# Optimization experiments

Measured on AMD Instinct MI355X. Metric: run time of the kernel, lower is better.

## Reference

```python
import jax, jax.numpy as jnp
import numpy as np

NB_FEATURES = 128
ACCUMULATION = 4


def iterative_inv(mat, n_iter=6):
    # Newton-Schulz iteration for matrix inverse ('original' init: global max)
    I = jnp.eye(mat.shape[-1], dtype=mat.dtype)
    K = mat
    V = (1.0 / jnp.max(jnp.sum(K, axis=-2))) * jnp.swapaxes(K, -1, -2)
    for _ in range(n_iter):
        KV = K @ V
        V = 0.25 * V @ (13.0 * I - KV @ (15.0 * I - KV @ (7.0 * I - KV)))
    return V


def setup_inputs() -> dict:
    key = jax.random.key(0)
    kq, kk, kv, ks = jax.random.split(key, 4)
    b, h, n, d = 4, 8, 2048, 64
    q = jax.random.normal(kq, (b, h, n, d), dtype=jnp.float32)
    k = jax.random.normal(kk, (b, h, n, d), dtype=jnp.float32)
    v = jax.random.normal(kv, (b, h, n, d), dtype=jnp.float32)
    mask = jnp.ones((b, n), dtype=jnp.float32)
    total = ACCUMULATION * NB_FEATURES
    # uniform_sketching: indices in [0,n) scaled by non_padding_num (=n here),
    # second half of the flat index list offset by +n to index the k-block of X.
    S = jax.random.randint(ks, (b, total), 0, n)
    S = S.at[:, total // 2:].add(n)
    sketching_matrix = S.reshape(b, ACCUMULATION, NB_FEATURES)
    random_sign = jnp.ones((b, ACCUMULATION, NB_FEATURES), dtype=jnp.float32)
    return {"q": q, "k": k, "v": v, "mask": mask,
            "random_sign": random_sign, "sketching_matrix": sketching_matrix}


def reference(q, k, v, mask, random_sign, sketching_matrix):
    b, h, n, d = q.shape
    data_normalizer = 32.0 ** (-0.25)
    m = mask[:, None, :, None]                      # [b,1,n,1]
    q = q * (m * data_normalizer)
    k = k * (m * data_normalizer)
    v = v * m

    X = jnp.concatenate([q, k], axis=2)             # [b,h,2n,d]
    Xt = jnp.transpose(X, (0, 2, 1, 3))             # [b,2n,h,d]
    XS = Xt[jnp.arange(b)[:, None, None], sketching_matrix]  # [b,acc,f,h,d]
    XS = jnp.transpose(XS, (0, 3, 1, 2, 4))         # [b,h,acc,f,d]

    # RS-RBF kernel sketch: exp(x.y - |x|^2/2 - |y|^2/2), accumulated over acc
    diag1 = (0.5 * jnp.sum(X * X, axis=-1))[:, :, None, :, None]   # [b,h,1,2n,1]
    diag2 = (0.5 * jnp.sum(XS * XS, axis=-1))[:, :, :, None, :]    # [b,h,acc,1,f]
    prod = jnp.einsum('bhnp,bhmfp->bhmnf', X, XS) - diag1 - diag2  # [b,h,acc,2n,f]
    res = jnp.exp(prod)
    res = jnp.transpose(res, (0, 1, 3, 2, 4))       # [b,h,2n,acc,f]
    AS = jnp.einsum('bhnmf,bmf->bhnf', res, random_sign)  # [b,h,2n,f]

    Q = AS[:, :, :n]                                # [b,h,n,f]
    K = AS[:, :, n:]                                # [b,h,n,f]

    ASt = jnp.transpose(AS, (0, 2, 1, 3))           # [b,2n,h,f]
    STAS = ASt[jnp.arange(b)[:, None, None], sketching_matrix]     # [b,acc,f,h,f]
    STAS = jnp.einsum('bmdhe,bmd->bhde', STAS, random_sign)        # [b,h,f,f]
    f = STAS.shape[-1]
    STAS = STAS + 0.1 * jnp.eye(f, dtype=STAS.dtype)

    D_inv = jnp.sqrt(1.0 / jnp.sum(STAS, axis=-1))  # [b,h,f]
    STAS_n = D_inv[..., :, None] * STAS * D_inv[..., None, :]
    STAS_inv = iterative_inv(STAS_n, 6)

    K = (K * D_inv[:, :, None, :]) @ STAS_inv       # [b,h,n,f]
    K = K * D_inv[:, :, None, :] * m

    context = jnp.einsum('bhnf,bhne->bhfe', K, v)   # [b,h,f,d]
    out = Q @ context                               # [b,h,n,d]
    return out
```

## Files before the change

kernel.cpp:

```cpp
#include <hip/hip_runtime.h>

constexpr int Bc = 4, Hc = 8, Nc = 2048, Dc = 64, Fc = 128, Mc = 4;
constexpr int BHc = Bc*Hc;
constexpr int T2c = 2*Nc;
constexpr int Jc  = Mc*Fc;
constexpr float DNORM = 0.4204482076268573f;

constexpr size_t OFF_AS    = 0;
constexpr size_t OFF_XSH   = OFF_AS    + (size_t)BHc*T2c*Fc;
constexpr size_t OFF_XSM   = OFF_XSH   + (size_t)BHc*Jc*Dc/2;
constexpr size_t OFF_XSL   = OFF_XSM   + (size_t)BHc*Jc*Dc/2;
constexpr size_t OFF_DIAG1 = OFF_XSL   + (size_t)BHc*Jc*Dc/2;
constexpr size_t OFF_DIAG2 = OFF_DIAG1 + (size_t)BHc*T2c;
constexpr size_t OFF_STASN = OFF_DIAG2 + (size_t)BHc*Jc;
constexpr size_t OFF_VBUF  = OFF_STASN + (size_t)BHc*Fc*Fc;
constexpr size_t OFF_DINV  = OFF_VBUF  + (size_t)BHc*Fc*Fc;
constexpr size_t OFF_GMAX  = OFF_DINV  + (size_t)BHc*Fc;
constexpr size_t OFF_CTX   = OFF_GMAX  + 64;
constexpr size_t OFF_KH    = OFF_CTX   + (size_t)BHc*Fc*Dc;
constexpr size_t OFF_KM    = OFF_KH    + (size_t)BHc*Fc*Fc/2;
constexpr size_t OFF_KL    = OFF_KM    + (size_t)BHc*Fc*Fc/2;
constexpr size_t OFF_GPART = OFF_XSH;
constexpr size_t OFF_ZSC   = OFF_GPART + (size_t)BHc*4*128*64;

typedef __attribute__((ext_vector_type(8))) short bf16x8;
typedef __attribute__((ext_vector_type(4))) float f32x4;
typedef __attribute__((ext_vector_type(4))) unsigned short u16x4;

__device__ __forceinline__ unsigned short f2bf_rne(float x) {
  unsigned int u = __float_as_uint(x);
  u += 0x7fff + ((u >> 16) & 1);
  return (unsigned short)(u >> 16);
}
__device__ __forceinline__ float bf2f(unsigned short h) {
  return __uint_as_float(((unsigned int)h) << 16);
}

__global__ __launch_bounds__(256) void diag1_kernel(
    const float* __restrict__ q, const float* __restrict__ k,
    const float* __restrict__ mask, float* __restrict__ diag1) {
  int gid = blockIdx.x*256 + threadIdx.x;
  int kq  = gid & 15;
  int row = gid >> 4;
  int t   = row & (T2c - 1);
  int bh  = row >> 12;
  int b   = bh >> 3;
  int tn  = (t < Nc) ? t : t - Nc;
  const float* src = ((t < Nc) ? q : k) + ((size_t)bh*Nc + tn)*Dc;
  float sc = DNORM * mask[b*Nc + tn];
  float4 x = *(const float4*)(src + kq*4);
  float s = x.x*x.x + x.y*x.y + x.z*x.z + x.w*x.w;
  s += __shfl_xor(s, 1);
  s += __shfl_xor(s, 2);
  s += __shfl_xor(s, 4);
  s += __shfl_xor(s, 8);
  if (kq == 0) diag1[row] = 0.5f * sc * sc * s;
}

__global__ __launch_bounds__(256) void gather_kernel(
    const float* __restrict__ q, const float* __restrict__ k,
    const float* __restrict__ mask, const int* __restrict__ sketch,
    const float* __restrict__ diag1,
    unsigned short* __restrict__ xsh, unsigned short* __restrict__ xsm,
    unsigned short* __restrict__ xsl, float* __restrict__ diag2) {
  int gid = blockIdx.x*256 + threadIdx.x;
  int kq  = gid & 15;
  int idx = gid >> 4;
  int j   = idx & (Jc - 1);
  int bh  = idx >> 9;
  int b   = bh >> 3;
  int t   = sketch[b*Jc + j];
  int tn  = (t < Nc) ? t : t - Nc;
  const float* src = ((t < Nc) ? q : k) + ((size_t)bh*Nc + tn)*Dc;
  float sc = DNORM * mask[b*Nc + tn];
  float4 x = *(const float4*)(src + kq*4);
  float xv[4] = {x.x*sc, x.y*sc, x.z*sc, x.w*sc};
  u16x4 hh, mm_, ll;
  #pragma unroll
  for (int jj = 0; jj < 4; ++jj) {
    unsigned short h = f2bf_rne(xv[jj]);
    float r1 = xv[jj] - bf2f(h);
    unsigned short m = f2bf_rne(r1);
    float r2 = r1 - bf2f(m);
    hh[jj] = h; mm_[jj] = m; ll[jj] = f2bf_rne(r2);
  }
  *(u16x4*)(xsh + (size_t)idx*Dc + kq*4) = hh;
  *(u16x4*)(xsm + (size_t)idx*Dc + kq*4) = mm_;
  *(u16x4*)(xsl + (size_t)idx*Dc + kq*4) = ll;
  if (kq == 0) diag2[idx] = diag1[bh*T2c + t];
}

__global__ __launch_bounds__(256) void as_mfma_kernel(
    const float* __restrict__ q, const float* __restrict__ k,
    const float* __restrict__ mask,
    const unsigned short* __restrict__ xsh, const unsigned short* __restrict__ xsm,
    const unsigned short* __restrict__ xsl,
    const float* __restrict__ diag1, const float* __restrict__ diag2,
    const float* __restrict__ sign, float* __restrict__ AS) {
  __shared__ __align__(16) unsigned short Ah[64][72];
  __shared__ __align__(16) unsigned short Am[64][72];
  __shared__ __align__(16) unsigned short Al[64][72];
  __shared__ float d1s[64];
  __shared__ float d2s[4][128];
  __shared__ float sgs[4][128];
  int bh = blockIdx.y, b = bh >> 3;
  int t0 = blockIdx.x * 64;
  int tid = threadIdx.x;
  int lane = tid & 63, wid = tid >> 6;
  int wr = wid >> 1, wc = wid & 1;
  int l16 = lane & 15, lg = lane >> 4;
  int R0 = wr*32, C0 = wc*64;

  for (int i = tid; i < 64*16; i += 256) {
    int r = i >> 4, kq = i & 15;
    int t = t0 + r;
    int tn = (t < Nc) ? t : t - Nc;
    const float* src = ((t < Nc) ? q : k) + ((size_t)bh*Nc + tn)*Dc + kq*4;
    float sc = DNORM * mask[b*Nc + tn];
    float4 x = *(const float4*)src;
    float xv[4] = {x.x*sc, x.y*sc, x.z*sc, x.w*sc};
    u16x4 hv, mv, lv;
    #pragma unroll
    for (int jj = 0; jj < 4; ++jj) {
      unsigned short h = f2bf_rne(xv[jj]);
      float r1 = xv[jj] - bf2f(h);
      unsigned short m = f2bf_rne(r1);
      float r2 = r1 - bf2f(m);
      hv[jj] = h; mv[jj] = m; lv[jj] = f2bf_rne(r2);
    }
    *(u16x4*)&Ah[r][kq*4] = hv;
    *(u16x4*)&Am[r][kq*4] = mv;
    *(u16x4*)&Al[r][kq*4] = lv;
  }
  if (tid < 64) d1s[tid] = diag1[bh*T2c + t0 + tid];
  for (int i = tid; i < 512; i += 256) {
    d2s[i>>7][i&127] = diag2[bh*Jc + i];
    sgs[i>>7][i&127] = sign[b*Jc + i];
  }
  __syncthreads();

  const unsigned short* xhh = xsh + (size_t)bh*Jc*Dc;
  const unsigned short* xmm = xsm + (size_t)bh*Jc*Dc;
  const unsigned short* xll = xsl + (size_t)bh*Jc*Dc;
  f32x4 oa[2][4];
  #pragma unroll
  for (int m = 0; m < 2; ++m)
    #pragma unroll
    for (int n = 0; n < 4; ++n) oa[m][n] = 0.f;

  for (int m = 0; m < Mc; ++m) {
    f32x4 acc[2][4];
    #pragma unroll
    for (int mm = 0; mm < 2; ++mm)
      #pragma unroll
      for (int nn = 0; nn < 4; ++nn) acc[mm][nn] = 0.f;
    #pragma unroll
    for (int kc = 0; kc < Dc; kc += 32) {
      int ko = kc + lg*8;
      bf16x8 ah[2], am2[2], al2[2], bhv[4], bmv[4], blv[4];
      #pragma unroll
      for (int mm = 0; mm < 2; ++mm) {
        ah[mm]  = *(const bf16x8*)&Ah[R0+16*mm+l16][ko];
        am2[mm] = *(const bf16x8*)&Am[R0+16*mm+l16][ko];
        al2[mm] = *(const bf16x8*)&Al[R0+16*mm+l16][ko];
      }
      #pragma unroll
      for (int nn = 0; nn < 4; ++nn) {
        size_t p = (size_t)(m*Fc + C0 + 16*nn + l16)*Dc + ko;
        bhv[nn] = *(const bf16x8*)(xhh + p);
        bmv[nn] = *(const bf16x8*)(xmm + p);
        blv[nn] = *(const bf16x8*)(xll + p);
      }
      #pragma unroll
      for (int mm = 0; mm < 2; ++mm)
        #pragma unroll
        for (int nn = 0; nn < 4; ++nn) {
          acc[mm][nn] = __builtin_amdgcn_mfma_f32_16x16x32_bf16(am2[mm], bmv[nn], acc[mm][nn], 0,0,0);
          acc[mm][nn] = __builtin_amdgcn_mfma_f32_16x16x32_bf16(ah[mm],  blv[nn], acc[mm][nn], 0,0,0);
          acc[mm][nn] = __builtin_amdgcn_mfma_f32_16x16x32_bf16(al2[mm], bhv[nn], acc[mm][nn], 0,0,0);
          acc[mm][nn] = __builtin_amdgcn_mfma_f32_16x16x32_bf16(ah[mm],  bmv[nn], acc[mm][nn], 0,0,0);
          acc[mm][nn] = __builtin_amdgcn_mfma_f32_16x16x32_bf16(am2[mm], bhv[nn], acc[mm][nn], 0,0,0);
          acc[mm][nn] = __builtin_amdgcn_mfma_f32_16x16x32_bf16(ah[mm],  bhv[nn], acc[mm][nn], 0,0,0);
        }
    }
    #pragma unroll
    for (int mm = 0; mm < 2; ++mm)
      #pragma unroll
      for (int nn = 0; nn < 4; ++nn) {
        int c = C0 + 16*nn + l16;
        float d2v = d2s[m][c], sg = sgs[m][c];
        #pragma unroll
        for (int r = 0; r < 4; ++r) {
          int row = R0 + 16*mm + 4*lg + r;
          oa[mm][nn][r] += sg * __expf(acc[mm][nn][r] - d1s[row] - d2v);
        }
      }
  }
  #pragma unroll
  for (int mm = 0; mm < 2; ++mm)
    #pragma unroll
    for (int nn = 0; nn < 4; ++nn) {
      int c = C0 + 16*nn + l16;
      #pragma unroll
      for (int r = 0; r < 4; ++r) {
        int row = R0 + 16*mm + 4*lg + r;
        AS[((size_t)bh*T2c + t0 + row)*Fc + c] = oa[mm][nn][r];
      }
    }
}

__global__ __launch_bounds__(256) void stas_kernel(
    const float* __restrict__ AS, const int* __restrict__ sketch,
    const float* __restrict__ sign,
    float* __restrict__ STASn, float* __restrict__ Dinv,
    unsigned short* __restrict__ Kh, unsigned short* __restrict__ Km,
    unsigned short* __restrict__ Kl,
    unsigned int* __restrict__ gmax) {
  extern __shared__ float stas[];
  __shared__ int   Ssh[Jc];
  __shared__ float sgn[Jc];
  __shared__ float Dl[Fc];
  __shared__ float red[Fc];
  int bh = blockIdx.x;
  int b  = bh >> 3;
  int tid = threadIdx.x;
  for (int i = tid; i < Jc; i += 256) {
    Ssh[i] = sketch[b*Jc + i];
    sgn[i] = sign[b*Jc + i];
  }
  __syncthreads();
  for (int i = tid; i < Fc*Fc; i += 256) {
    int dd = i >> 7, e = i & 127;
    float vsum = 0.f;
    #pragma unroll
    for (int m = 0; m < Mc; ++m) {
      int t = Ssh[m*Fc + dd];
      vsum += sgn[m*Fc + dd] * AS[((size_t)bh*T2c + t)*Fc + e];
    }
    if (dd == e) vsum += 0.1f;
    stas[dd*129 + e] = vsum;
  }
  __syncthreads();
  if (tid < Fc) {
    float s = 0.f;
    for (int e = 0; e < Fc; ++e) s += stas[tid*129 + e];
    float di = 1.0f / sqrtf(s);
    Dl[tid] = di;
    Dinv[bh*Fc + tid] = di;
  }
  __syncthreads();
  for (int i = tid; i < Fc*Fc; i += 256) {
    int dd = i >> 7, e = i & 127;
    float vv = stas[dd*129 + e] * Dl[dd] * Dl[e];
    stas[dd*129 + e] = vv;
    STASn[(size_t)bh*Fc*Fc + i] = vv;
    unsigned short hb = f2bf_rne(vv); float r1 = vv - bf2f(hb);
    unsigned short mb = f2bf_rne(r1); float r2 = r1 - bf2f(mb);
    Kh[(size_t)bh*Fc*Fc + i] = hb;
    Km[(size_t)bh*Fc*Fc + i] = mb;
    Kl[(size_t)bh*Fc*Fc + i] = f2bf_rne(r2);
  }
  __syncthreads();
  if (tid < Fc) {
    float s = 0.f;
    for (int dd = 0; dd < Fc; ++dd) s += stas[dd*129 + tid];
    red[tid] = s;
  }
  __syncthreads();
  if (tid == 0) {
    float mx = 0.f;
    for (int e = 0; e < Fc; ++e) mx = fmaxf(mx, red[e]);
    atomicMax(gmax, __float_as_uint(mx));
  }
}

__device__ __forceinline__ unsigned boff(int brow, int ke) {
  unsigned byte = ((unsigned)brow << 8) | ((unsigned)ke << 1);
  return byte ^ (((unsigned)(brow & 7)) << 4);
}

__device__ __forceinline__ void mm6(const bf16x8 ah[2], const bf16x8 am[2], const bf16x8 al[2],
                                    const bf16x8 bh[4], const bf16x8 bm[4], const bf16x8 bl[4],
                                    f32x4 acc[2][4]) {
  #pragma unroll
  for (int m = 0; m < 2; ++m)
    #pragma unroll
    for (int n = 0; n < 4; ++n) {
      acc[m][n] = __builtin_amdgcn_mfma_f32_16x16x32_bf16(am[m], bm[n], acc[m][n], 0,0,0);
      acc[m][n] = __builtin_amdgcn_mfma_f32_16x16x32_bf16(ah[m], bl[n], acc[m][n], 0,0,0);
      acc[m][n] = __builtin_amdgcn_mfma_f32_16x16x32_bf16(al[m], bh[n], acc[m][n], 0,0,0);
      acc[m][n] = __builtin_amdgcn_mfma_f32_16x16x32_bf16(ah[m], bm[n], acc[m][n], 0,0,0);
      acc[m][n] = __builtin_amdgcn_mfma_f32_16x16x32_bf16(am[m], bh[n], acc[m][n], 0,0,0);
      acc[m][n] = __builtin_amdgcn_mfma_f32_16x16x32_bf16(ah[m], bh[n], acc[m][n], 0,0,0);
    }
}

__device__ __forceinline__ void ld3(const char* Ph, const char* Pm, const char* Pl,
                                    int brow, int ko, bf16x8& h, bf16x8& m, bf16x8& l) {
  unsigned off = boff(brow, ko);
  h = *(const bf16x8*)(Ph + off);
  m = *(const bf16x8*)(Pm + off);
  l = *(const bf16x8*)(Pl + off);
}

__device__ __forceinline__ void mm_p1(
    const unsigned short* __restrict__ kh, const unsigned short* __restrict__ km,
    const unsigned short* __restrict__ kl,
    const char* Ah, const char* Am, const char* Al,
    int R0, int C0, int l16, int lg, f32x4 acc[2][4]) {
  #pragma unroll 1
  for (int kc = 0; kc < Fc; kc += 32) {
    int ko = kc + lg*8;
    bf16x8 ah[2], am[2], al[2], bh[4], bm[4], bl[4];
    #pragma unroll
    for (int m = 0; m < 2; ++m) {
      size_t p = (size_t)(R0+16*m+l16)*Fc + ko;
      ah[m] = *(const bf16x8*)(kh + p);
      am[m] = *(const bf16x8*)(km + p);
      al[m] = *(const bf16x8*)(kl + p);
    }
    #pragma unroll
    for (int n = 0; n < 4; ++n)
      ld3(Ah, Am, Al, C0+16*n+l16, ko, bh[n], bm[n], bl[n]);
    mm6(ah, am, al, bh, bm, bl, acc);
  }
}

__device__ __forceinline__ void mm_p234(
    const char* Ah, const char* Am, const char* Al,
    const char* Zh, const char* Zm, const unsigned short* __restrict__ ZlG,
    int R0, int C0, int l16, int lg, f32x4 acc[2][4]) {
  #pragma unroll 1
  for (int kc = 0; kc < Fc; kc += 32) {
    int ko = kc + lg*8;
    bf16x8 ah[2], am[2], al[2], bh[4], bm[4], bl[4];
    #pragma unroll
    for (int m = 0; m < 2; ++m)
      ld3(Ah, Am, Al, R0+16*m+l16, ko, ah[m], am[m], al[m]);
    #pragma unroll
    for (int n = 0; n < 4; ++n) {
      int col = C0+16*n+l16;
      unsigned off = boff(col, ko);
      bh[n] = *(const bf16x8*)(Zh + off);
      bm[n] = *(const bf16x8*)(Zm + off);
      bl[n] = *(const bf16x8*)(ZlG + col*Fc + ko);
    }
    mm6(ah, am, al, bh, bm, bl, acc);
  }
}

__device__ __forceinline__ void split4(f32x4 v, u16x4& hv, u16x4& mv, u16x4& lv) {
  #pragma unroll
  for (int r = 0; r < 4; ++r) {
    unsigned short hb = f2bf_rne(v[r]); float r1 = v[r] - bf2f(hb);
    unsigned short mb = f2bf_rne(r1);   float r2 = r1 - bf2f(mb);
    hv[r] = hb; mv[r] = mb; lv[r] = f2bf_rne(r2);
  }
}
__device__ __forceinline__ void wbA3(char* Ah, char* Am, char* Al,
                                     int col, int row0, f32x4 v) {
  u16x4 hv, mv, lv;
  split4(v, hv, mv, lv);
  unsigned off = boff(col, row0);
  *(u16x4*)(Ah + off) = hv;
  *(u16x4*)(Am + off) = mv;
  *(u16x4*)(Al + off) = lv;
}
__device__ __forceinline__ void wbZ3(char* Zh, char* Zm, unsigned short* __restrict__ ZlG,
                                     int col, int row0, f32x4 v) {
  u16x4 hv, mv, lv;
  split4(v, hv, mv, lv);
  unsigned off = boff(col, row0);
  *(u16x4*)(Zh + off) = hv;
  *(u16x4*)(Zm + off) = mv;
  *(u16x4*)(ZlG + col*Fc + row0) = lv;
}

__global__ __launch_bounds__(512) void newton_ctx_kernel(
    const float* __restrict__ STASn,
    const unsigned short* __restrict__ KhG, const unsigned short* __restrict__ KmG,
    const unsigned short* __restrict__ KlG,
    const float* __restrict__ gmaxf, float* __restrict__ Vout,
    const float* __restrict__ ASg, const float* __restrict__ vg,
    const float* __restrict__ maskg, float* __restrict__ Gpart,
    unsigned short* __restrict__ ZlScr) {
  extern __shared__ char smc[];
  int tid  = threadIdx.x;

  if (blockIdx.x < BHc) {
    char* Ah = smc;
    char* Am = smc + 32768;
    char* Al = smc + 65536;
    char* Zh = smc + 98304;
    char* Zm = smc + 131072;
    int bh = blockIdx.x;
    const float* Kp = STASn + (size_t)bh*Fc*Fc;
    const unsigned short* kh = KhG + (size_t)bh*Fc*Fc;
    const unsigned short* km = KmG + (size_t)bh*Fc*Fc;
    const unsigned short* kl = KlG + (size_t)bh*Fc*Fc;
    unsigned short* ZlG = ZlScr + (size_t)bh*Fc*Fc;
    float ginv = 1.0f / gmaxf[0];
    int lane = tid & 63;
    int wid  = tid >> 6;
    int wr = wid >> 1, wc = wid & 1;
    int l16 = lane & 15, lg = lane >> 4;
    int R0 = wr*32, C0 = wc*64;
    int drow0 = lg*4;

    f32x4 vreg[2][4];
    #pragma unroll
    for (int m = 0; m < 2; ++m)
      #pragma unroll
      for (int n = 0; n < 4; ++n) {
        int col = C0 + 16*n + l16;
        #pragma unroll
        for (int r = 0; r < 4; ++r)
          vreg[m][n][r] = Kp[(size_t)(R0 + 16*m + drow0 + r)*Fc + col] * ginv;
        wbA3(Ah, Am, Al, col, R0 + 16*m + drow0, vreg[m][n]);
      }
    __syncthreads();

    f32x4 fin[2][4];
    for (int it = 0; it < 6; ++it) {
      f32x4 acc[2][4];
      #pragma unroll
      for (int m = 0; m < 2; ++m) for (int n = 0; n < 4; ++n) acc[m][n] = 0.f;
      mm_p1(kh, km, kl, Ah, Am, Al, R0, C0, l16, lg, acc);
      #pragma unroll
      for (int m = 0; m < 2; ++m)
        #pragma unroll
        for (int n = 0; n < 4; ++n)
          wbZ3(Zh, Zm, ZlG, C0 + 16*n + l16, R0 + 16*m + drow0, acc[m][n]);
      __syncthreads();

      #pragma unroll
      for (int m = 0; m < 2; ++m) for (int n = 0; n < 4; ++n) acc[m][n] = 0.f;
      mm_p234(Ah, Am, Al, Zh, Zm, ZlG, R0, C0, l16, lg, acc);
      #pragma unroll
      for (int m = 0; m < 2; ++m)
        #pragma unroll
        for (int n = 0; n < 4; ++n)
          fin[m][n] = 13.f*vreg[m][n] - 15.f*acc[m][n];
      __syncthreads();
      #pragma unroll
      for (int m = 0; m < 2; ++m)
        #pragma unroll
        for (int n = 0; n < 4; ++n)
          wbA3(Ah, Am, Al, C0 + 16*n + l16, R0 + 16*m + drow0, acc[m][n]);
      __syncthreads();

      #pragma unroll
      for (int m = 0; m < 2; ++m) for (int n = 0; n < 4; ++n) acc[m][n] = 0.f;
      mm_p234(Ah, Am, Al, Zh, Zm, ZlG, R0, C0, l16, lg, acc);
      #pragma unroll
      for (int m = 0; m < 2; ++m)
        #pragma unroll
        for (int n = 0; n < 4; ++n)
          fin[m][n] += 7.f*acc[m][n];
      __syncthreads();
      #pragma unroll
      for (int m = 0; m < 2; ++m)
        #pragma unroll
        for (int n = 0; n < 4; ++n)
          wbA3(Ah, Am, Al, C0 + 16*n + l16, R0 + 16*m + drow0, acc[m][n]);
      __syncthreads();

      #pragma unroll
      for (int m = 0; m < 2; ++m) for (int n = 0; n < 4; ++n) acc[m][n] = 0.f;
      mm_p234(Ah, Am, Al, Zh, Zm, ZlG, R0, C0, l16, lg, acc);
      #pragma unroll
      for (int m = 0; m < 2; ++m)
        #pragma unroll
        for (int n = 0; n < 4; ++n) {
          fin[m][n] = 0.25f*(fin[m][n] - acc[m][n]);
          vreg[m][n] = fin[m][n];
        }
      __syncthreads();
      #pragma unroll
      for (int m = 0; m < 2; ++m)
        #pragma unroll
        for (int n = 0; n < 4; ++n)
          wbA3(Ah, Am, Al, C0 + 16*n + l16, R0 + 16*m + drow0, fin[m][n]);
      __syncthreads();
    }

    float* Vo = Vout + (size_t)bh*Fc*Fc;
    #pragma unroll
    for (int m = 0; m < 2; ++m)
      #pragma unroll
      for (int n = 0; n < 4; ++n) {
        int col = C0 + 16*n + l16;
        #pragma unroll
        for (int r = 0; r < 4; ++r)
          Vo[(size_t)(R0 + 16*m + drow0 + r)*Fc + col] = vreg[m][n][r];
      }
  } else {
    float* Ksh = (float*)smc;
    float* vsh = (float*)(smc + 32768);
    int id = blockIdx.x - BHc;
    int cbh = id >> 2, chunk = id & 3;
    int cb = cbh >> 3;
    int t0 = chunk * 512;
    int f = tid & 127, g = tid >> 7;
    float acc[16];
    #pragma unroll
    for (int j = 0; j < 16; ++j) acc[j] = 0.f;
    for (int sub = 0; sub < 8; ++sub) {
      __syncthreads();
      int ts = t0 + sub*64;
      for (int i = tid; i < 64*32; i += 512) {
        int r = i >> 5, c4 = i & 31;
        *(float4*)&Ksh[r*128 + c4*4] =
            *(const float4*)(ASg + ((size_t)cbh*T2c + Nc + ts + r)*Fc + c4*4);
      }
      for (int i = tid; i < 64*16; i += 512) {
        int r = i >> 4, c4 = i & 15;
        float mk = maskg[cb*Nc + ts + r];
        float m2 = mk*mk;
        float4 x = *(const float4*)(vg + ((size_t)cbh*Nc + ts + r)*Dc + c4*4);
        x.x*=m2; x.y*=m2; x.z*=m2; x.w*=m2;
        *(float4*)&vsh[r*64 + c4*4] = x;
      }
      __syncthreads();
      #pragma unroll 2
      for (int tl = 0; tl < 64; ++tl) {
        float kf = Ksh[tl*128 + f];
        #pragma unroll
        for (int j4 = 0; j4 < 4; ++j4) {
          float4 vv = *(const float4*)&vsh[tl*64 + g*16 + j4*4];
          acc[j4*4+0] += kf*vv.x; acc[j4*4+1] += kf*vv.y;
          acc[j4*4+2] += kf*vv.z; acc[j4*4+3] += kf*vv.w;
        }
      }
    }
    float* gp = Gpart + ((((size_t)cbh*4 + chunk)*128 + f)*64 + g*16);
    #pragma unroll
    for (int j4 = 0; j4 < 4; ++j4)
      *(float4*)(gp + j4*4) = *(const float4*)&acc[j4*4];
  }
}

__global__ __launch_bounds__(256) void ctx_fix_kernel(
    const float* __restrict__ Gpart, const float* __restrict__ Vinv,
    const float* __restrict__ Dinv, float* __restrict__ ctxo) {
  __shared__ float DG[128*64];
  __shared__ float Dl[128];
  int bh = blockIdx.x;
  int tid = threadIdx.x;
  if (tid < 128) Dl[tid] = Dinv[bh*Fc + tid];
  __syncthreads();
  for (int i = tid; i < 2048; i += 256) {
    int e = i >> 4, c4 = i & 15;
    const float* g0 = Gpart + ((((size_t)bh*4)*128 + e)*64 + c4*4);
    float4 s0 = *(const float4*)(g0);
    float4 s1 = *(const float4*)(g0 + 8192);
    float4 s2 = *(const float4*)(g0 + 16384);
    float4 s3 = *(const float4*)(g0 + 24576);
    float de = Dl[e];
    float4 o;
    o.x = (s0.x+s1.x+s2.x+s3.x)*de;
    o.y = (s0.y+s1.y+s2.y+s3.y)*de;
    o.z = (s0.z+s1.z+s2.z+s3.z)*de;
    o.w = (s0.w+s1.w+s2.w+s3.w)*de;
    *(float4*)&DG[e*64 + c4*4] = o;
  }
  __syncthreads();
  int f = tid & 127, half = tid >> 7;
  float acc[32];
  #pragma unroll
  for (int j = 0; j < 32; ++j) acc[j] = 0.f;
  for (int e = 0; e < 128; ++e) {
    float s = Vinv[(size_t)bh*Fc*Fc + (size_t)e*Fc + f];
    #pragma unroll
    for (int j4 = 0; j4 < 8; ++j4) {
      float4 dg = *(const float4*)&DG[e*64 + half*32 + j4*4];
      acc[j4*4+0] += s*dg.x; acc[j4*4+1] += s*dg.y;
      acc[j4*4+2] += s*dg.z; acc[j4*4+3] += s*dg.w;
    }
  }
  float df = Dl[f];
  float* op = ctxo + (size_t)bh*Fc*Dc + f*Dc + half*32;
  #pragma unroll
  for (int j4 = 0; j4 < 8; ++j4) {
    float4 o;
    o.x = acc[j4*4+0]*df; o.y = acc[j4*4+1]*df;
    o.z = acc[j4*4+2]*df; o.w = acc[j4*4+3]*df;
    *(float4*)(op + j4*4) = o;
  }
}

__global__ __launch_bounds__(256) void out_kernel(
    const float* __restrict__ AS, const float* __restrict__ ctx,
    float* __restrict__ out) {
  extern __shared__ float smo[];
  float* Asq = smo;
  float* Cs  = smo + 64*132;
  int bh = blockIdx.y;
  int row0 = blockIdx.x * 64;
  int tid = threadIdx.x;
  int tr = tid >> 4, tc = tid & 15;
  for (int i = tid; i < 64*32; i += 256) {
    int r = i >> 5, kq = i & 31;
    *(float4*)&Asq[r*132 + kq*4] =
        *(const float4*)(AS + ((size_t)bh*T2c + row0 + r)*Fc + kq*4);
  }
  for (int i = tid; i < 128*16; i += 256) {
    int r = i >> 4, kq = i & 15;
    *(float4*)&Cs[r*64 + kq*4] =
        *(const float4*)(ctx + (size_t)bh*Fc*Dc + r*Dc + kq*4);
  }
  __syncthreads();
  float acc[4][4] = {};
  #pragma unroll 2
  for (int kk = 0; kk < Fc; ++kk) {
    float4 bv = *(const float4*)&Cs[kk*64 + tc*4];
    float a0 = Asq[(tr*4+0)*132 + kk];
    float a1 = Asq[(tr*4+1)*132 + kk];
    float a2 = Asq[(tr*4+2)*132 + kk];
    float a3 = Asq[(tr*4+3)*132 + kk];
    acc[0][0] += a0*bv.x; acc[0][1] += a0*bv.y; acc[0][2] += a0*bv.z; acc[0][3] += a0*bv.w;
    acc[1][0] += a1*bv.x; acc[1][1] += a1*bv.y; acc[1][2] += a1*bv.z; acc[1][3] += a1*bv.w;
    acc[2][0] += a2*bv.x; acc[2][1] += a2*bv.y; acc[2][2] += a2*bv.z; acc[2][3] += a2*bv.w;
    acc[3][0] += a3*bv.x; acc[3][1] += a3*bv.y; acc[3][2] += a3*bv.z; acc[3][3] += a3*bv.w;
  }
  #pragma unroll
  for (int i = 0; i < 4; ++i) {
    float4 o;
    o.x = acc[i][0]; o.y = acc[i][1]; o.z = acc[i][2]; o.w = acc[i][3];
    *(float4*)(out + ((size_t)bh*Nc + row0 + tr*4 + i)*Dc + tc*4) = o;
  }
}

extern "C" void kernel_launch(void* const* d_in, const int* in_sizes, int n_in,
                              void* d_out, int out_size, void* d_ws, size_t ws_size,
                              hipStream_t stream) {
  const float* q    = (const float*)d_in[0];
  const float* k    = (const float*)d_in[1];
  const float* v    = (const float*)d_in[2];
  const float* mask = (const float*)d_in[3];
  const float* sign = (const float*)d_in[4];
  const int*   sketch = (const int*)d_in[5];
  float* out = (float*)d_out;
  float* ws  = (float*)d_ws;

  unsigned short* xsh = (unsigned short*)(ws + OFF_XSH);
  unsigned short* xsm = (unsigned short*)(ws + OFF_XSM);
  unsigned short* xsl = (unsigned short*)(ws + OFF_XSL);
  unsigned short* kh  = (unsigned short*)(ws + OFF_KH);
  unsigned short* km  = (unsigned short*)(ws + OFF_KM);
  unsigned short* kl  = (unsigned short*)(ws + OFF_KL);
  unsigned short* zsc = (unsigned short*)(ws + OFF_ZSC);

  hipMemsetAsync(ws + OFF_GMAX, 0, sizeof(float), stream);

  diag1_kernel<<<BHc*T2c*16/256, 256, 0, stream>>>(q, k, mask, ws + OFF_DIAG1);
  gather_kernel<<<BHc*Jc*16/256, 256, 0, stream>>>(q, k, mask, sketch, ws + OFF_DIAG1,
                                                   xsh, xsm, xsl, ws + OFF_DIAG2);
  as_mfma_kernel<<<dim3(T2c/64, BHc), 256, 0, stream>>>(q, k, mask, xsh, xsm, xsl,
      ws + OFF_DIAG1, ws + OFF_DIAG2, sign, ws + OFF_AS);
  stas_kernel<<<BHc, 256, 128*129*sizeof(float), stream>>>(ws + OFF_AS, sketch, sign,
      ws + OFF_STASN, ws + OFF_DINV, kh, km, kl, (unsigned int*)(ws + OFF_GMAX));
  newton_ctx_kernel<<<BHc + 128, 512, 163840, stream>>>(ws + OFF_STASN, kh, km, kl,
      ws + OFF_GMAX, ws + OFF_VBUF, ws + OFF_AS, v, mask, ws + OFF_GPART, zsc);
  ctx_fix_kernel<<<BHc, 256, 0, stream>>>(ws + OFF_GPART, ws + OFF_VBUF,
      ws + OFF_DINV, ws + OFF_CTX);
  out_kernel<<<dim3(Nc/64, BHc), 256, (64*132 + 128*64)*sizeof(float), stream>>>(
      ws + OFF_AS, ws + OFF_CTX, out);
}
```

Before: 359.6 us.

## Use split-bf16 MFMA for output matmul and cache Z-high fragments in Newton loop

```diff
diff --git a/kernel.cpp b/kernel.cpp
--- a/kernel.cpp
+++ b/kernel.cpp
@@ -308,7 +308,7 @@
     const unsigned short* __restrict__ kl,
     const char* Ah, const char* Am, const char* Al,
     int R0, int C0, int l16, int lg, f32x4 acc[2][4]) {
-  #pragma unroll 1
+  #pragma unroll 2
   for (int kc = 0; kc < Fc; kc += 32) {
     int ko = kc + lg*8;
     bf16x8 ah[2], am[2], al[2], bh[4], bm[4], bl[4];
@@ -326,13 +326,14 @@
   }
 }
 
-__device__ __forceinline__ void mm_p234(
+__device__ __forceinline__ void mm_p2(
     const char* Ah, const char* Am, const char* Al,
     const char* Zh, const char* Zm, const unsigned short* __restrict__ ZlG,
+    bf16x8 (&zch)[4][4],
     int R0, int C0, int l16, int lg, f32x4 acc[2][4]) {
-  #pragma unroll 1
-  for (int kc = 0; kc < Fc; kc += 32) {
-    int ko = kc + lg*8;
+  #pragma unroll
+  for (int kc = 0; kc < 4; ++kc) {
+    int ko = kc*32 + lg*8;
     bf16x8 ah[2], am[2], al[2], bh[4], bm[4], bl[4];
     #pragma unroll
     for (int m = 0; m < 2; ++m)
@@ -343,6 +344,30 @@
       unsigned off = boff(col, ko);
       bh[n] = *(const bf16x8*)(Zh + off);
       bm[n] = *(const bf16x8*)(Zm + off);
+      bl[n] = *(const bf16x8*)(ZlG + col*Fc + ko);
+      zch[kc][n] = bh[n];
+    }
+    mm6(ah, am, al, bh, bm, bl, acc);
+  }
+}
+
+__device__ __forceinline__ void mm_p34(
+    const char* Ah, const char* Am, const char* Al,
+    const char* Zm, const unsigned short* __restrict__ ZlG,
+    const bf16x8 (&zch)[4][4],
+    int R0, int C0, int l16, int lg, f32x4 acc[2][4]) {
+  #pragma unroll
+  for (int kc = 0; kc < 4; ++kc) {
+    int ko = kc*32 + lg*8;
+    bf16x8 ah[2], am[2], al[2], bh[4], bm[4], bl[4];
+    #pragma unroll
+    for (int m = 0; m < 2; ++m)
+      ld3(Ah, Am, Al, R0+16*m+l16, ko, ah[m], am[m], al[m]);
+    #pragma unroll
+    for (int n = 0; n < 4; ++n) {
+      int col = C0+16*n+l16;
+      bh[n] = zch[kc][n];
+      bm[n] = *(const bf16x8*)(Zm + boff(col, ko));
       bl[n] = *(const bf16x8*)(ZlG + col*Fc + ko);
     }
     mm6(ah, am, al, bh, bm, bl, acc);
@@ -376,7 +401,7 @@
   *(u16x4*)(ZlG + col*Fc + row0) = lv;
 }
 
-__global__ __launch_bounds__(512) void newton_ctx_kernel(
+__global__ __launch_bounds__(512, 2) void newton_ctx_kernel(
     const float* __restrict__ STASn,
     const unsigned short* __restrict__ KhG, const unsigned short* __restrict__ KmG,
     const unsigned short* __restrict__ KlG,
@@ -421,6 +446,7 @@
     __syncthreads();
 
     f32x4 fin[2][4];
+    bf16x8 zch[4][4];
     for (int it = 0; it < 6; ++it) {
       f32x4 acc[2][4];
       #pragma unroll
@@ -435,7 +461,7 @@
 
       #pragma unroll
       for (int m = 0; m < 2; ++m) for (int n = 0; n < 4; ++n) acc[m][n] = 0.f;
-      mm_p234(Ah, Am, Al, Zh, Zm, ZlG, R0, C0, l16, lg, acc);
+      mm_p2(Ah, Am, Al, Zh, Zm, ZlG, zch, R0, C0, l16, lg, acc);
       #pragma unroll
       for (int m = 0; m < 2; ++m)
         #pragma unroll
@@ -451,7 +477,7 @@
 
       #pragma unroll
       for (int m = 0; m < 2; ++m) for (int n = 0; n < 4; ++n) acc[m][n] = 0.f;
-      mm_p234(Ah, Am, Al, Zh, Zm, ZlG, R0, C0, l16, lg, acc);
+      mm_p34(Ah, Am, Al, Zm, ZlG, zch, R0, C0, l16, lg, acc);
       #pragma unroll
       for (int m = 0; m < 2; ++m)
         #pragma unroll
@@ -467,7 +493,7 @@
 
       #pragma unroll
       for (int m = 0; m < 2; ++m) for (int n = 0; n < 4; ++n) acc[m][n] = 0.f;
-      mm_p234(Ah, Am, Al, Zh, Zm, ZlG, R0, C0, l16, lg, acc);
+      mm_p34(Ah, Am, Al, Zm, ZlG, zch, R0, C0, l16, lg, acc);
       #pragma unroll
       for (int m = 0; m < 2; ++m)
         #pragma unroll
@@ -589,46 +615,85 @@
   }
 }
 
-__global__ __launch_bounds__(256) void out_kernel(
+__global__ __launch_bounds__(256) void out_mfma_kernel(
     const float* __restrict__ AS, const float* __restrict__ ctx,
     float* __restrict__ out) {
-  extern __shared__ float smo[];
-  float* Asq = smo;
-  float* Cs  = smo + 64*132;
+  extern __shared__ char smo[];
+  char* Qh = smo;
+  char* Qm = smo + 16384;
+  char* Ql = smo + 32768;
+  char* Ch = smo + 49152;
+  char* Cm = smo + 65536;
+  char* Cl = smo + 81920;
   int bh = blockIdx.y;
   int row0 = blockIdx.x * 64;
   int tid = threadIdx.x;
-  int tr = tid >> 4, tc = tid & 15;
-  for (int i = tid; i < 64*32; i += 256) {
+  int lane = tid & 63, wid = tid >> 6;
+  int wr = wid >> 1, wc = wid & 1;
+  int l16 = lane & 15, lg = lane >> 4;
+  int R0 = wr*32, C0 = wc*32;
+
+  for (int i = tid; i < 2048; i += 256) {
     int r = i >> 5, kq = i & 31;
-    *(float4*)&Asq[r*132 + kq*4] =
-        *(const float4*)(AS + ((size_t)bh*T2c + row0 + r)*Fc + kq*4);
-  }
-  for (int i = tid; i < 128*16; i += 256) {
-    int r = i >> 4, kq = i & 15;
-    *(float4*)&Cs[r*64 + kq*4] =
-        *(const float4*)(ctx + (size_t)bh*Fc*Dc + r*Dc + kq*4);
-  }
-  __syncthreads();
-  float acc[4][4] = {};
-  #pragma unroll 2
-  for (int kk = 0; kk < Fc; ++kk) {
-    float4 bv = *(const float4*)&Cs[kk*64 + tc*4];
-    float a0 = Asq[(tr*4+0)*132 + kk];
-    float a1 = Asq[(tr*4+1)*132 + kk];
-    float a2 = Asq[(tr*4+2)*132 + kk];
-    float a3 = Asq[(tr*4+3)*132 + kk];
-    acc[0][0] += a0*bv.x; acc[0][1] += a0*bv.y; acc[0][2] += a0*bv.z; acc[0][3] += a0*bv.w;
-    acc[1][0] += a1*bv.x; acc[1][1] += a1*bv.y; acc[1][2] += a1*bv.z; acc[1][3] += a1*bv.w;
-    acc[2][0] += a2*bv.x; acc[2][1] += a2*bv.y; acc[2][2] += a2*bv.z; acc[2][3] += a2*bv.w;
-    acc[3][0] += a3*bv.x; acc[3][1] += a3*bv.y; acc[3][2] += a3*bv.z; acc[3][3] += a3*bv.w;
-  }
-  #pragma unroll
-  for (int i = 0; i < 4; ++i) {
-    float4 o;
-    o.x = acc[i][0]; o.y = acc[i][1]; o.z = acc[i][2]; o.w = acc[i][3];
-    *(float4*)(out + ((size_t)bh*Nc + row0 + tr*4 + i)*Dc + tc*4) = o;
-  }
+    f32x4 x = *(const f32x4*)(AS + ((size_t)bh*T2c + row0 + r)*Fc + kq*4);
+    u16x4 hv, mv, lv;
+    split4(x, hv, mv, lv);
+    unsigned off = boff(r, kq*4);
+    *(u16x4*)(Qh + off) = hv;
+    *(u16x4*)(Qm + off) = mv;
+    *(u16x4*)(Ql + off) = lv;
+  }
+  for (int i = tid; i < 2048; i += 256) {
+    int c = i >> 5, e4 = i & 31;
+    f32x4 x;
+    #pragma unroll
+    for (int j = 0; j < 4; ++j)
+      x[j] = ctx[(size_t)bh*Fc*Dc + (size_t)(e4*4+j)*Dc + c];
+    u16x4 hv, mv, lv;
+    split4(x, hv, mv, lv);
+    unsigned off = boff(c, e4*4);
+    *(u16x4*)(Ch + off) = hv;
+    *(u16x4*)(Cm + off) = mv;
+    *(u16x4*)(Cl + off) = lv;
+  }
+  __syncthreads();
+
+  f32x4 acc[2][2];
+  #pragma unroll
+  for (int m = 0; m < 2; ++m)
+    #pragma unroll
+    for (int n = 0; n < 2; ++n) acc[m][n] = 0.f;
+  #pragma unroll
+  for (int kc = 0; kc < 4; ++kc) {
+    int ko = kc*32 + lg*8;
+    bf16x8 ah[2], am[2], al[2], bh2[2], bm2[2], bl2[2];
+    #pragma unroll
+    for (int m = 0; m < 2; ++m)
+      ld3(Qh, Qm, Ql, R0+16*m+l16, ko, ah[m], am[m], al[m]);
+    #pragma unroll
+    for (int n = 0; n < 2; ++n)
+      ld3(Ch, Cm, Cl, C0+16*n+l16, ko, bh2[n], bm2[n], bl2[n]);
+    #pragma unroll
+    for (int m = 0; m < 2; ++m)
+      #pragma unroll
+      for (int n = 0; n < 2; ++n) {
+        acc[m][n] = __builtin_amdgcn_mfma_f32_16x16x32_bf16(am[m], bm2[n], acc[m][n], 0,0,0);
+        acc[m][n] = __builtin_amdgcn_mfma_f32_16x16x32_bf16(ah[m], bl2[n], acc[m][n], 0,0,0);
+        acc[m][n] = __builtin_amdgcn_mfma_f32_16x16x32_bf16(al[m], bh2[n], acc[m][n], 0,0,0);
+        acc[m][n] = __builtin_amdgcn_mfma_f32_16x16x32_bf16(ah[m], bm2[n], acc[m][n], 0,0,0);
+        acc[m][n] = __builtin_amdgcn_mfma_f32_16x16x32_bf16(am[m], bh2[n], acc[m][n], 0,0,0);
+        acc[m][n] = __builtin_amdgcn_mfma_f32_16x16x32_bf16(ah[m], bh2[n], acc[m][n], 0,0,0);
+      }
+  }
+  #pragma unroll
+  for (int m = 0; m < 2; ++m)
+    #pragma unroll
+    for (int n = 0; n < 2; ++n) {
+      int col = C0 + 16*n + l16;
+      #pragma unroll
+      for (int r = 0; r < 4; ++r)
+        out[((size_t)bh*Nc + row0 + R0 + 16*m + lg*4 + r)*Dc + col] = acc[m][n][r];
+    }
 }
 
 extern "C" void kernel_launch(void* const* d_in, const int* in_sizes, int n_in,
@@ -664,6 +729,6 @@
       ws + OFF_GMAX, ws + OFF_VBUF, ws + OFF_AS, v, mask, ws + OFF_GPART, zsc);
   ctx_fix_kernel<<<BHc, 256, 0, stream>>>(ws + OFF_GPART, ws + OFF_VBUF,
       ws + OFF_DINV, ws + OFF_CTX);
-  out_kernel<<<dim3(Nc/64, BHc), 256, (64*132 + 128*64)*sizeof(float), stream>>>(
+  out_mfma_kernel<<<dim3(Nc/64, BHc), 256, 98304, stream>>>(
       ws + OFF_AS, ws + OFF_CTX, out);
 }
```

Measured after the change: 408.0 us. +13.5%, slower.
